# Kernel optimization log

Measured on AMD Instinct MI355X. Metric: run time of the kernel, lower is better.

## Reference

```python
import jax, jax.numpy as jnp
import numpy as np

B, N, D = 256, 8192, 768
TEMP = 0.05          # CE temperature (temp init arg; CE losses are computed but NOT returned)
SUPCON_T = 0.07      # standard SupConLoss temperature (default in the repo's SupConLoss)


def _l2norm(x, eps=1e-12):
    # matches F.normalize(dim=-1): clamp of the norm by eps
    n = jnp.linalg.norm(x, axis=-1, keepdims=True)
    return x / jnp.maximum(n, eps)


def _supcon(feats, mem, labels, mem_labels):
    # SupConLoss(features, memory, targets, prototype_labels):
    # anchor-vs-memory logits, positives where labels match prototype labels.
    logits = feats @ mem.T / SUPCON_T                              # [B, N]
    logits = logits - jax.lax.stop_gradient(logits.max(axis=1, keepdims=True))
    log_prob = logits - jax.nn.logsumexp(logits, axis=1, keepdims=True)
    mask = (labels[:, None] == mem_labels[None, :]).astype(logits.dtype)
    mean_log_prob_pos = (mask * log_prob).sum(1) / jnp.maximum(mask.sum(1), 1.0)
    return -mean_log_prob_pos.mean()


def setup_inputs() -> dict:
    key = jax.random.key(0)
    k1, k2, k3, k4, k5, k6, k7, k8 = jax.random.split(key, 8)
    inputs_rgb = jax.random.normal(k1, (B, D), dtype=jnp.float32)
    inputs_ir = jax.random.normal(k2, (B, D), dtype=jnp.float32)
    targets_rgb = jax.random.randint(k3, (B,), 0, N)
    targets_ir = jax.random.randint(k4, (B,), 0, N)
    # memory banks are unit-normalized prototypes in practice
    features_rgb = _l2norm(jax.random.normal(k5, (N, D), dtype=jnp.float32))
    features_ir = _l2norm(jax.random.normal(k6, (N, D), dtype=jnp.float32))
    # prototype labels: permutations of arange(N) so cross-modal lookups always match
    prototype_labels_rgb = jax.random.permutation(k7, jnp.arange(N))
    prototype_labels_ir = jax.random.permutation(k8, jnp.arange(N))
    return {
        "inputs_rgb": inputs_rgb, "inputs_ir": inputs_ir,
        "targets_rgb": targets_rgb, "targets_ir": targets_ir,
        "features_rgb": features_rgb, "features_ir": features_ir,
        "prototype_labels_rgb": prototype_labels_rgb,
        "prototype_labels_ir": prototype_labels_ir,
    }


def reference(inputs_rgb, inputs_ir, targets_rgb, targets_ir,
              features_rgb, features_ir, prototype_labels_rgb, prototype_labels_ir):
    x_rgb = _l2norm(inputs_rgb)
    x_ir = _l2norm(inputs_ir)
    # cm_double forward matmuls -> CE losses are computed in torch but never returned
    # (dead w.r.t. the module's outputs), so they don't affect the returned values.
    loss_contr = (_supcon(x_rgb, features_rgb, targets_rgb, prototype_labels_rgb)
                  + _supcon(x_ir, features_ir, targets_ir, prototype_labels_ir))
    loss_contr_cross = (_supcon(x_rgb, features_ir, targets_rgb, prototype_labels_ir)
                        + _supcon(x_ir, features_rgb, targets_ir, prototype_labels_rgb))
    return (loss_contr, loss_contr_cross)
```

## Files before the change

kernel.cpp:

```cpp
#include <hip/hip_runtime.h>
#include <hip/hip_bf16.h>
#include <math.h>

#define Bsz 256
#define Nsz 8192
#define Dsz 768
#define NROWS 512
#define INV_T 14.2857142857f
#define NT 64
#define NCB (Nsz / NT)
#define KC 64
#define NSTG (Dsz / KC)

typedef __attribute__((ext_vector_type(4))) float f32x4;
typedef __attribute__((ext_vector_type(8))) short bf16x8;
typedef __attribute__((ext_vector_type(4))) short bf16x4;

__device__ __forceinline__ unsigned short f2bf(float f) {
    union { float f; unsigned u; } x; x.f = f;
    unsigned u = x.u;
    return (unsigned short)((u + 0x7fffu + ((u >> 16) & 1u)) >> 16);
}
__device__ __forceinline__ float bf2f(unsigned short u) {
    union { unsigned u; float f; } x; x.u = ((unsigned)u) << 16;
    return x.f;
}

__device__ __forceinline__ void barrier_lgkm() {
    asm volatile("s_waitcnt lgkmcnt(0)" ::: "memory");
    __builtin_amdgcn_s_barrier();
    asm volatile("" ::: "memory");
}

__device__ __forceinline__ int fr_idx(int row, int k) {
    int rb = row >> 4, kc = k >> 5;
    int lane = (((k >> 3) & 3) << 4) | (row & 15);
    return (((rb * 24 + kc) << 6) | lane) * 8 + (k & 7);
}

__device__ __forceinline__ bf16x8 cvt8(float4 a, float4 b) {
    union { bf16x8 v; __hip_bfloat162 h[4]; } r;
    r.h[0] = __float22bfloat162_rn({a.x, a.y});
    r.h[1] = __float22bfloat162_rn({a.z, a.w});
    r.h[2] = __float22bfloat162_rn({b.x, b.y});
    r.h[3] = __float22bfloat162_rn({b.z, b.w});
    return r.v;
}

__global__ void k_prep(const float* __restrict__ xrgb, const float* __restrict__ xir,
                       const int* __restrict__ prgb, const int* __restrict__ pir,
                       unsigned short* __restrict__ xrm, unsigned short* __restrict__ xfr,
                       int* __restrict__ inv, float* __restrict__ out) {
    int b = blockIdx.x, t = threadIdx.x;
    if (b == 0 && t < 2) out[t] = 0.0f;
    if (b < NROWS) {
        const float* src = (b < Bsz) ? (xrgb + b * Dsz) : (xir + (b - Bsz) * Dsz);
        float v0 = src[t], v1 = src[t + 256], v2 = src[t + 512];
        float ss = v0 * v0 + v1 * v1 + v2 * v2;
        #pragma unroll
        for (int m = 1; m < 64; m <<= 1) ss += __shfl_xor(ss, m);
        __shared__ float w4[4];
        if ((t & 63) == 0) w4[t >> 6] = ss;
        __syncthreads();
        float tot = w4[0] + w4[1] + w4[2] + w4[3];
        float invn = 1.0f / fmaxf(sqrtf(tot), 1e-12f);
        unsigned short b0 = f2bf(v0 * invn), b1 = f2bf(v1 * invn), b2 = f2bf(v2 * invn);
        xrm[b * Dsz + t] = b0;
        xrm[b * Dsz + t + 256] = b1;
        xrm[b * Dsz + t + 512] = b2;
        xfr[fr_idx(b, t)] = b0;
        xfr[fr_idx(b, t + 256)] = b1;
        xfr[fr_idx(b, t + 512)] = b2;
    } else {
        int i = (b - NROWS) * 256 + t;
        if (i < Nsz) inv[prgb[i]] = i;
        else         inv[Nsz + pir[i - Nsz]] = i - Nsz;
    }
}

__global__ __launch_bounds__(512) void k_big(
    const float* __restrict__ Frgb, const float* __restrict__ Fir,
    const unsigned short* __restrict__ xfr,
    float* __restrict__ part_m, float* __restrict__ part_s) {
    __shared__ short Bs[2][NT * KC];
    int bid = blockIdx.x;
    int bank = bid >> 7;
    int cb = bid & (NCB - 1);
    const float* F = bank ? Fir : Frgb;
    int t = threadIdx.x;
    int w = t >> 6, lane = t & 63, lr = lane & 15, lg = lane >> 4;

    int scol = t >> 3, sj = t & 7;
    const float* sbase = F + (long)(cb * NT + scol) * Dsz + sj * 8;
    int swidx = scol * 64 + ((sj * 8) ^ ((scol & 7) << 3));

    f32x4 acc[4][4] = {};

    float4 u0 = *(const float4*)sbase;
    float4 v0 = *(const float4*)(sbase + 4);
    float4 u1 = *(const float4*)(sbase + KC);
    float4 v1 = *(const float4*)(sbase + KC + 4);
    *(bf16x8*)&Bs[0][swidx] = cvt8(u0, v0);
    barrier_lgkm();

    bf16x8 a0[4], a1[4];
    #pragma unroll
    for (int rf = 0; rf < 4; ++rf)
        a0[rf] = *(const bf16x8*)&xfr[((((w * 4 + rf) * 24 + 0) << 6) | lane) * 8];

    for (int s = 0; s < NSTG; ++s) {
        if (s + 2 < NSTG) {
            const float* p = sbase + (s + 2) * KC;
            if ((s & 1) == 0) { u0 = *(const float4*)p; v0 = *(const float4*)(p + 4); }
            else              { u1 = *(const float4*)p; v1 = *(const float4*)(p + 4); }
        }
        const short* B0 = Bs[s & 1];
        {
            int kcn = s * 2 + 1;
            #pragma unroll
            for (int rf = 0; rf < 4; ++rf)
                a1[rf] = *(const bf16x8*)&xfr[((((w * 4 + rf) * 24 + kcn) << 6) | lane) * 8];
            bf16x8 bfr[4];
            #pragma unroll
            for (int cf = 0; cf < 4; ++cf) {
                int col = cf * 16 + lr;
                int kloc = lg * 8;
                bfr[cf] = *(const bf16x8*)&B0[col * 64 + (kloc ^ ((col & 7) << 3))];
            }
            #pragma unroll
            for (int rf = 0; rf < 4; ++rf)
                #pragma unroll
                for (int cf = 0; cf < 4; ++cf)
                    acc[rf][cf] = __builtin_amdgcn_mfma_f32_16x16x32_bf16(a0[rf], bfr[cf], acc[rf][cf], 0, 0, 0);
        }
        {
            int kcn = s * 2 + 2;
            if (kcn < 2 * NSTG) {
                #pragma unroll
                for (int rf = 0; rf < 4; ++rf)
                    a0[rf] = *(const bf16x8*)&xfr[((((w * 4 + rf) * 24 + kcn) << 6) | lane) * 8];
            }
            bf16x8 bfr[4];
            #pragma unroll
            for (int cf = 0; cf < 4; ++cf) {
                int col = cf * 16 + lr;
                int kloc = 32 + lg * 8;
                bfr[cf] = *(const bf16x8*)&B0[col * 64 + (kloc ^ ((col & 7) << 3))];
            }
            #pragma unroll
            for (int rf = 0; rf < 4; ++rf)
                #pragma unroll
                for (int cf = 0; cf < 4; ++cf)
                    acc[rf][cf] = __builtin_amdgcn_mfma_f32_16x16x32_bf16(a1[rf], bfr[cf], acc[rf][cf], 0, 0, 0);
        }
        if (s + 1 < NSTG) {
            if (((s + 1) & 1) == 0) *(bf16x8*)&Bs[0][swidx] = cvt8(u0, v0);
            else                    *(bf16x8*)&Bs[1][swidx] = cvt8(u1, v1);
        }
        barrier_lgkm();
    }

    #pragma unroll
    for (int rf = 0; rf < 4; ++rf) {
        #pragma unroll
        for (int reg = 0; reg < 4; ++reg) {
            float p0 = acc[rf][0][reg] * INV_T, p1 = acc[rf][1][reg] * INV_T;
            float p2 = acc[rf][2][reg] * INV_T, p3 = acc[rf][3][reg] * INV_T;
            float mx = fmaxf(fmaxf(p0, p1), fmaxf(p2, p3));
            mx = fmaxf(mx, __shfl_xor(mx, 1));
            mx = fmaxf(mx, __shfl_xor(mx, 2));
            mx = fmaxf(mx, __shfl_xor(mx, 4));
            mx = fmaxf(mx, __shfl_xor(mx, 8));
            float sum = __expf(p0 - mx) + __expf(p1 - mx) + __expf(p2 - mx) + __expf(p3 - mx);
            sum += __shfl_xor(sum, 1); sum += __shfl_xor(sum, 2);
            sum += __shfl_xor(sum, 4); sum += __shfl_xor(sum, 8);
            if (lr == 0) {
                int row = w * 64 + rf * 16 + lg * 4 + reg;
                long o = (long)(bank * NROWS + row) * NCB + cb;
                part_m[o] = mx;
                part_s[o] = sum;
            }
        }
    }
}

__global__ void k_combine(const float* __restrict__ part_m, const float* __restrict__ part_s,
                          const float* __restrict__ Frgb, const float* __restrict__ Fir,
                          const int* __restrict__ trgb, const int* __restrict__ tir,
                          const unsigned short* __restrict__ xrm, const int* __restrict__ inv,
                          float* __restrict__ out) {
    int gw = (blockIdx.x * blockDim.x + threadIdx.x) >> 6;
    int lane = threadIdx.x & 63;
    int wl = threadIdx.x >> 6;
    int bank = gw >> 9, r = gw & 511;
    const float* pm = part_m + (long)(bank * NROWS + r) * NCB;
    const float* ps = part_s + (long)(bank * NROWS + r) * NCB;
    float m1 = pm[lane], m2 = pm[lane + 64];
    float s1 = ps[lane], s2 = ps[lane + 64];
    float m = fmaxf(m1, m2);
    float s = s1 * __expf(m1 - m) + s2 * __expf(m2 - m);
    #pragma unroll
    for (int mm = 32; mm; mm >>= 1) {
        float om = __shfl_xor(m, mm), os = __shfl_xor(s, mm);
        float nm = fmaxf(m, om);
        s = s * __expf(m - nm) + os * __expf(om - nm);
        m = nm;
    }
    int tgt = (r < Bsz) ? trgb[r] : tir[r - Bsz];
    int j = inv[bank * Nsz + tgt];
    const float* frow = (bank ? Fir : Frgb) + (long)j * Dsz;
    const unsigned short* xrow = xrm + r * Dsz;
    float d = 0.0f;
    #pragma unroll
    for (int p = 0; p < 3; ++p) {
        int k = p * 256 + lane * 4;
        bf16x4 xv = *(const bf16x4*)&xrow[k];
        float4 fv = *(const float4*)&frow[k];
        d += bf2f((unsigned short)xv[0]) * fv.x + bf2f((unsigned short)xv[1]) * fv.y
           + bf2f((unsigned short)xv[2]) * fv.z + bf2f((unsigned short)xv[3]) * fv.w;
    }
    #pragma unroll
    for (int mm = 1; mm < 64; mm <<= 1) d += __shfl_xor(d, mm);

    __shared__ float red[4];
    if (lane == 0) red[wl] = (m + __logf(s)) - d * INV_T;
    __syncthreads();
    if (threadIdx.x == 0) {
        int seg = bank ^ ((r >= Bsz) ? 1 : 0);
        float tot = (red[0] + red[1] + red[2] + red[3]) * (1.0f / 256.0f);
        atomicAdd(&out[seg], tot);
    }
}

extern "C" void kernel_launch(void* const* d_in, const int* in_sizes, int n_in,
                              void* d_out, int out_size, void* d_ws, size_t ws_size,
                              hipStream_t stream) {
    const float* in_rgb = (const float*)d_in[0];
    const float* in_ir  = (const float*)d_in[1];
    const int*   t_rgb  = (const int*)d_in[2];
    const int*   t_ir   = (const int*)d_in[3];
    const float* F_rgb  = (const float*)d_in[4];
    const float* F_ir   = (const float*)d_in[5];
    const int*   p_rgb  = (const int*)d_in[6];
    const int*   p_ir   = (const int*)d_in[7];
    float* out = (float*)d_out;
    char* ws = (char*)d_ws;

    unsigned short* xrm = (unsigned short*)ws;
    unsigned short* xfr = (unsigned short*)(ws + 786432);
    int*   inv    = (int*)  (ws + 1572864);
    float* part_m = (float*)(ws + 1638400);
    float* part_s = (float*)(ws + 2162688);

    k_prep   <<<NROWS + 64, 256, 0, stream>>>(in_rgb, in_ir, p_rgb, p_ir, xrm, xfr, inv, out);
    k_big    <<<2 * NCB, 512, 0, stream>>>(F_rgb, F_ir, xfr, part_m, part_s);
    k_combine<<<256, 256, 0, stream>>>(part_m, part_s, F_rgb, F_ir, t_rgb, t_ir, xrm, inv, out);
}
```

Measured before the change: 124.4 us.

## Split k_big row tiles across two blocks of 256 threads each

Each k_big block now covers half of the 512 anchor rows with 4 waves instead of 8, so the grid doubles to 512 blocks. The staging pattern changes so each of the 256 threads loads 16 floats of the memory-bank tile, and __launch_bounds__(256,2) is set. The aim is to spread work across more CUs and improve occupancy and latency hiding. The cost is that every memory-bank tile is read from global memory and converted to bf16 twice, once per row half.

After: 123.8 us. Within noise of the previous version (-0.5%).

```diff
diff --git a/kernel.cpp b/kernel.cpp
--- a/kernel.cpp
+++ b/kernel.cpp
@@ -78,48 +78,58 @@
     }
 }
 
-__global__ __launch_bounds__(512) void k_big(
+__global__ __launch_bounds__(256, 2) void k_big(
     const float* __restrict__ Frgb, const float* __restrict__ Fir,
     const unsigned short* __restrict__ xfr,
     float* __restrict__ part_m, float* __restrict__ part_s) {
     __shared__ short Bs[2][NT * KC];
     int bid = blockIdx.x;
-    int bank = bid >> 7;
-    int cb = bid & (NCB - 1);
+    int bank = bid >> 8;
+    int rh   = (bid >> 7) & 1;
+    int cb   = bid & (NCB - 1);
     const float* F = bank ? Fir : Frgb;
     int t = threadIdx.x;
     int w = t >> 6, lane = t & 63, lr = lane & 15, lg = lane >> 4;
 
-    int scol = t >> 3, sj = t & 7;
-    const float* sbase = F + (long)(cb * NT + scol) * Dsz + sj * 8;
-    int swidx = scol * 64 + ((sj * 8) ^ ((scol & 7) << 3));
+    int scol = t >> 2, sj = t & 3;
+    const float* sbase = F + (long)(cb * NT + scol) * Dsz + sj * 16;
+    int sw0 = scol * 64 + ((sj * 16)     ^ ((scol & 7) << 3));
+    int sw1 = scol * 64 + ((sj * 16 + 8) ^ ((scol & 7) << 3));
 
     f32x4 acc[4][4] = {};
 
-    float4 u0 = *(const float4*)sbase;
-    float4 v0 = *(const float4*)(sbase + 4);
-    float4 u1 = *(const float4*)(sbase + KC);
-    float4 v1 = *(const float4*)(sbase + KC + 4);
-    *(bf16x8*)&Bs[0][swidx] = cvt8(u0, v0);
+    float4 u0[4], u1[4];
+    #pragma unroll
+    for (int j = 0; j < 4; ++j) u0[j] = *(const float4*)(sbase + j * 4);
+    #pragma unroll
+    for (int j = 0; j < 4; ++j) u1[j] = *(const float4*)(sbase + KC + j * 4);
+    *(bf16x8*)&Bs[0][sw0] = cvt8(u0[0], u0[1]);
+    *(bf16x8*)&Bs[0][sw1] = cvt8(u0[2], u0[3]);
     barrier_lgkm();
 
+    int rbb = rh * 16 + w * 4;
     bf16x8 a0[4], a1[4];
     #pragma unroll
     for (int rf = 0; rf < 4; ++rf)
-        a0[rf] = *(const bf16x8*)&xfr[((((w * 4 + rf) * 24 + 0) << 6) | lane) * 8];
+        a0[rf] = *(const bf16x8*)&xfr[((((rbb + rf) * 24 + 0) << 6) | lane) * 8];
 
     for (int s = 0; s < NSTG; ++s) {
         if (s + 2 < NSTG) {
             const float* p = sbase + (s + 2) * KC;
-            if ((s & 1) == 0) { u0 = *(const float4*)p; v0 = *(const float4*)(p + 4); }
-            else              { u1 = *(const float4*)p; v1 = *(const float4*)(p + 4); }
+            if ((s & 1) == 0) {
+                #pragma unroll
+                for (int j = 0; j < 4; ++j) u0[j] = *(const float4*)(p + j * 4);
+            } else {
+                #pragma unroll
+                for (int j = 0; j < 4; ++j) u1[j] = *(const float4*)(p + j * 4);
+            }
         }
         const short* B0 = Bs[s & 1];
         {
             int kcn = s * 2 + 1;
             #pragma unroll
             for (int rf = 0; rf < 4; ++rf)
-                a1[rf] = *(const bf16x8*)&xfr[((((w * 4 + rf) * 24 + kcn) << 6) | lane) * 8];
+                a1[rf] = *(const bf16x8*)&xfr[((((rbb + rf) * 24 + kcn) << 6) | lane) * 8];
             bf16x8 bfr[4];
             #pragma unroll
             for (int cf = 0; cf < 4; ++cf) {
@@ -138,7 +148,7 @@
             if (kcn < 2 * NSTG) {
                 #pragma unroll
                 for (int rf = 0; rf < 4; ++rf)
-                    a0[rf] = *(const bf16x8*)&xfr[((((w * 4 + rf) * 24 + kcn) << 6) | lane) * 8];
+                    a0[rf] = *(const bf16x8*)&xfr[((((rbb + rf) * 24 + kcn) << 6) | lane) * 8];
             }
             bf16x8 bfr[4];
             #pragma unroll
@@ -154,8 +164,13 @@
                     acc[rf][cf] = __builtin_amdgcn_mfma_f32_16x16x32_bf16(a1[rf], bfr[cf], acc[rf][cf], 0, 0, 0);
         }
         if (s + 1 < NSTG) {
-            if (((s + 1) & 1) == 0) *(bf16x8*)&Bs[0][swidx] = cvt8(u0, v0);
-            else                    *(bf16x8*)&Bs[1][swidx] = cvt8(u1, v1);
+            if (((s + 1) & 1) == 0) {
+                *(bf16x8*)&Bs[0][sw0] = cvt8(u0[0], u0[1]);
+                *(bf16x8*)&Bs[0][sw1] = cvt8(u0[2], u0[3]);
+            } else {
+                *(bf16x8*)&Bs[1][sw0] = cvt8(u1[0], u1[1]);
+                *(bf16x8*)&Bs[1][sw1] = cvt8(u1[2], u1[3]);
+            }
         }
         barrier_lgkm();
     }
@@ -175,7 +190,7 @@
             sum += __shfl_xor(sum, 1); sum += __shfl_xor(sum, 2);
             sum += __shfl_xor(sum, 4); sum += __shfl_xor(sum, 8);
             if (lr == 0) {
-                int row = w * 64 + rf * 16 + lg * 4 + reg;
+                int row = rh * 256 + w * 64 + rf * 16 + lg * 4 + reg;
                 long o = (long)(bank * NROWS + row) * NCB + cb;
                 part_m[o] = mx;
                 part_s[o] = sum;
@@ -253,6 +268,6 @@
     float* part_s = (float*)(ws + 2162688);
 
     k_prep   <<<NROWS + 64, 256, 0, stream>>>(in_rgb, in_ir, p_rgb, p_ir, xrm, xfr, inv, out);
-    k_big    <<<2 * NCB, 512, 0, stream>>>(F_rgb, F_ir, xfr, part_m, part_s);
+    k_big    <<<4 * NCB, 256, 0, stream>>>(F_rgb, F_ir, xfr, part_m, part_s);
     k_combine<<<256, 256, 0, stream>>>(part_m, part_s, F_rgb, F_ir, t_rgb, t_ir, xrm, inv, out);
 }
```
